# Performance work log

Measured on AMD Instinct MI355X. Metric: run time of the kernel, lower is better.

The kernel has to match this reference:

```python
import jax, jax.numpy as jnp
import numpy as np

B, S, D = 2, 1024, 1024
NH = 8
QK = 512   # qk_dim = 0.5 * D
V = 1024   # v_dim = 1.0 * D
DQK = QK // NH   # 64
DHV = V // NH    # 128
CAP = 15.0       # gate_soft_cap
NORM_EPS = 1e-6
DENOM_EPS = 1e-6


def soft_cap(x, cap):
    return cap * jnp.tanh(x / cap)


def setup_inputs() -> dict:
    key = jax.random.key(0)
    ks = jax.random.split(key, 8)
    s = 0.02
    return {
        "x": jax.random.normal(ks[0], (B, S, D), jnp.float32),
        "Wq": jax.random.normal(ks[1], (QK, D), jnp.float32) * s,
        "Wk": jax.random.normal(ks[2], (QK, D), jnp.float32) * s,
        "Wv": jax.random.normal(ks[3], (V, D), jnp.float32) * s,
        "Wog": jax.random.normal(ks[4], (V, D), jnp.float32) * s,
        "Wi": jax.random.normal(ks[5], (NH, D), jnp.float32) * s,
        "bi": jnp.zeros((NH,), jnp.float32),
        "Wf": jax.random.normal(ks[6], (NH, D), jnp.float32) * s,
        "bf": jnp.ones((NH,), jnp.float32),  # positive forget bias
        "gamma": jnp.ones((V,), jnp.float32),
        "Wout": jax.random.normal(ks[7], (D, V), jnp.float32) * s,
    }


def _mlstm_recurrent(q, k, v, i_pre, f_pre):
    # q,k: [B,S,NH,DQK]; v: [B,S,NH,DHV]; i_pre,f_pre: [B,S,NH]
    f_log = jax.nn.log_sigmoid(f_pre)
    q_s = q * (DQK ** -0.5)
    # move time to leading axis for scan
    xs = (jnp.moveaxis(q_s, 1, 0), jnp.moveaxis(k, 1, 0), jnp.moveaxis(v, 1, 0),
          jnp.moveaxis(i_pre, 1, 0), jnp.moveaxis(f_log, 1, 0))
    C0 = jnp.zeros((B, NH, DQK, DHV), q.dtype)
    n0 = jnp.zeros((B, NH, DQK), q.dtype)
    m0 = jnp.zeros((B, NH), q.dtype)

    def step(carry, xt):
        C, n, m = carry
        qt, kt, vt, it, ft = xt  # [B,NH,*]
        m_new = jnp.maximum(ft + m, it)                      # [B,NH]
        f_act = jnp.exp(ft + m - m_new)
        i_act = jnp.exp(it - m_new)
        C = f_act[..., None, None] * C + i_act[..., None, None] * (kt[..., :, None] * vt[..., None, :])
        n = f_act[..., None] * n + i_act[..., None] * kt
        h_num = jnp.einsum('bhd,bhdv->bhv', qt, C)
        qn = jnp.einsum('bhd,bhd->bh', qt, n)
        denom = jnp.maximum(jnp.abs(qn), jnp.exp(-m_new)) + DENOM_EPS
        h = h_num / denom[..., None]
        return (C, n, m_new), h

    (C, n, m), hs = jax.lax.scan(step, (C0, n0, m0), xs)
    return jnp.moveaxis(hs, 0, 1), (C, n, m)  # h: [B,S,NH,DHV]


def reference(x, Wq, Wk, Wv, Wog, Wi, bi, Wf, bf, gamma, Wout):
    q = (x @ Wq.T).reshape(B, S, NH, DQK)
    k = (x @ Wk.T).reshape(B, S, NH, DQK)
    v = (x @ Wv.T).reshape(B, S, NH, DHV)
    o_pre = x @ Wog.T                                  # [B,S,V]
    i_pre = soft_cap(x @ Wi.T + bi, CAP)               # [B,S,NH]
    f_pre = soft_cap(x @ Wf.T + bf, CAP)               # [B,S,NH]

    h, _state = _mlstm_recurrent(q, k, v, i_pre, f_pre)  # [B,S,NH,DHV]

    # multi-head layernorm over head dim, float32 reductions
    h32 = h.astype(jnp.float32)
    mu = jnp.mean(h32, axis=-1, keepdims=True)
    var = jnp.mean(jnp.square(h32 - mu), axis=-1, keepdims=True)
    h_norm = ((h32 - mu) * jax.lax.rsqrt(var + NORM_EPS)).astype(h.dtype)
    h_norm = h_norm * gamma.reshape(NH, DHV)
    h_norm = h_norm.reshape(B, S, V)

    h_out = jax.nn.sigmoid(o_pre) * h_norm
    y = h_out @ Wout.T
    return y
```

## Files before the change

### kernel.cpp

```cpp
#include <hip/hip_runtime.h>
#include <hip/hip_bf16.h>
#include <math.h>

typedef __bf16 bf16x8 __attribute__((ext_vector_type(8)));
typedef float f32x4 __attribute__((ext_vector_type(4)));

#define NB 2
#define NS 1024
#define ND 1024
#define NH 8
#define NQK 512
#define NV 1024
#define DQK 64
#define DHV 128
#define CHUNK 64
#define NCHUNK 16

#define GLDS16(g, l) __builtin_amdgcn_global_load_lds((const __attribute__((address_space(1))) void*)(g), (__attribute__((address_space(3))) void*)(l), 16, 0, 0)

static __device__ __forceinline__ void split_bf16(float v, __bf16& hi, __bf16& lo) {
  hi = (__bf16)v;
  lo = (__bf16)(v - (float)hi);
}

__global__ __launch_bounds__(256) void cvt_all(const float* __restrict__ x,
    const float* __restrict__ wq, const float* __restrict__ wk,
    const float* __restrict__ wv, const float* __restrict__ wog,
    const float* __restrict__ wout,
    __bf16* __restrict__ xb, __bf16* __restrict__ wb, __bf16* __restrict__ wob) {
  long i = (long)blockIdx.x * 256 + threadIdx.x;
  const float* src; __bf16* dst;
  if (i < 524288)        { src = x    + i*4;                    dst = xb  + i*4; }
  else if (i < 655360)   { long j = i -  524288; src = wq  + j*4; dst = wb + j*4; }
  else if (i < 786432)   { long j = i -  655360; src = wk  + j*4; dst = wb +  524288 + j*4; }
  else if (i < 1048576)  { long j = i -  786432; src = wv  + j*4; dst = wb + 1048576 + j*4; }
  else if (i < 1310720)  { long j = i - 1048576; src = wog + j*4; dst = wb + 2097152 + j*4; }
  else                   { long j = i - 1310720; src = wout+ j*4; dst = wob + j*4; }
  float4 v = *(const float4*)src;
  __bf16 o[4];
  o[0] = (__bf16)v.x; o[1] = (__bf16)v.y; o[2] = (__bf16)v.z; o[3] = (__bf16)v.w;
  *(short4*)dst = *(const short4*)o;
}

__global__ __launch_bounds__(256) void gemm_bt(const __bf16* __restrict__ A,
                                               const __bf16* __restrict__ Bm,
                                               float* __restrict__ C,
                                               int M, int N, int K) {
  __shared__ __bf16 smA[128 * 64];
  __shared__ __bf16 smB[128 * 64];
  const int tid = threadIdx.x;
  const int m0 = blockIdx.y * 128;
  const int n0 = blockIdx.x * 128;
  const int wid = tid >> 6, lane = tid & 63;
  const int wm = (wid >> 1) * 64, wn = (wid & 1) * 64;
  const int fr = lane & 15;
  const int g  = lane >> 4;
  f32x4 acc[4][4] = {};
  for (int kt = 0; kt < K; kt += 64) {
    #pragma unroll
    for (int i = 0; i < 4; ++i) {
      const int sbase = i * 256 + wid * 64;
      const int s = sbase + lane;
      const int row = s >> 3;
      const int klog = (s & 7) ^ (row & 7);
      GLDS16(A  + (size_t)(m0 + row) * K + kt + klog * 8, smA + sbase * 8);
      GLDS16(Bm + (size_t)(n0 + row) * K + kt + klog * 8, smB + sbase * 8);
    }
    __syncthreads();
    #pragma unroll
    for (int kk = 0; kk < 2; ++kk) {
      const int kg = kk * 4 + g;
      bf16x8 af[4], bfv[4];
      #pragma unroll
      for (int f = 0; f < 4; ++f) {
        const int Ra = wm + f * 16 + fr;
        const int Rb = wn + f * 16 + fr;
        af[f]  = *(const bf16x8*)&smA[Ra * 64 + ((kg ^ (Ra & 7)) * 8)];
        bfv[f] = *(const bf16x8*)&smB[Rb * 64 + ((kg ^ (Rb & 7)) * 8)];
      }
      #pragma unroll
      for (int i = 0; i < 4; ++i)
        #pragma unroll
        for (int j = 0; j < 4; ++j)
          acc[i][j] = __builtin_amdgcn_mfma_f32_16x16x32_bf16(af[i], bfv[j], acc[i][j], 0, 0, 0);
    }
    __syncthreads();
  }
  const int orow = m0 + wm + g * 4;
  const int ocol = n0 + wn + fr;
  #pragma unroll
  for (int i = 0; i < 4; ++i)
    #pragma unroll
    for (int j = 0; j < 4; ++j)
      #pragma unroll
      for (int r = 0; r < 4; ++r)
        C[(size_t)(orow + i*16 + r) * N + (ocol + j*16)] = acc[i][j][r];
}

__global__ __launch_bounds__(256) void ifgate_kernel(const float* __restrict__ x,
    const float* __restrict__ Wi, const float* __restrict__ bi,
    const float* __restrict__ Wf, const float* __restrict__ bf_,
    float* __restrict__ icap, float* __restrict__ flog) {
  const int row = blockIdx.x;
  const int w = threadIdx.x >> 6;
  const int l = threadIdx.x & 63;
  const float* xr = x + (size_t)row * ND;
  float xv[16];
  #pragma unroll
  for (int t = 0; t < 16; ++t) xv[t] = xr[l + 64*t];
  for (int hh = 0; hh < 2; ++hh) {
    int h = w*2 + hh;
    const float* wi = Wi + (size_t)h * ND;
    const float* wf = Wf + (size_t)h * ND;
    float si = 0.f, sf = 0.f;
    #pragma unroll
    for (int t = 0; t < 16; ++t) {
      si += xv[t] * wi[l + 64*t];
      sf += xv[t] * wf[l + 64*t];
    }
    #pragma unroll
    for (int off = 32; off; off >>= 1) {
      si += __shfl_xor(si, off, 64);
      sf += __shfl_xor(sf, off, 64);
    }
    if (l == 0) {
      float ic = 15.f * tanhf((si + bi[h]) * (1.f/15.f));
      float fc = 15.f * tanhf((sf + bf_[h]) * (1.f/15.f));
      float fl = (fc >= 0.f) ? -log1pf(__expf(-fc)) : (fc - log1pf(__expf(fc)));
      icap[row*NH + h] = ic;
      flog[row*NH + h] = fl;
    }
  }
}

__global__ __launch_bounds__(64) void gates_kernel(const float* __restrict__ icap,
    const float* __restrict__ flog, float* __restrict__ g_g, float* __restrict__ a_g,
    float* __restrict__ m_g, float* __restrict__ m0g) {
  const int bh = blockIdx.x;
  const int b = bh >> 3, h = bh & 7;
  const int l = threadIdx.x;
  float m0 = 0.f;
  for (int c = 0; c < NCHUNK; ++c) {
    const int t = c*CHUNK + l;
    const int row = b*NS + t;
    float B = flog[row*NH + h];
    float iv = icap[row*NH + h];
    #pragma unroll
    for (int d = 1; d < 64; d <<= 1) {
      float o = __shfl_up(B, d, 64);
      if (l >= d) B += o;
    }
    float g = iv - B;
    float cm = g;
    #pragma unroll
    for (int d = 1; d < 64; d <<= 1) {
      float o = __shfl_up(cm, d, 64);
      if (l >= d) cm = fmaxf(cm, o);
    }
    float a = fmaxf(m0, cm);
    float m = B + a;
    const int idx = bh*NS + t;
    g_g[idx] = g; a_g[idx] = a; m_g[idx] = m;
    if (l == 0) m0g[bh*NCHUNK + c] = m0;
    m0 = __shfl(m, 63, 64);
  }
}

__global__ __launch_bounds__(256) void u_kernel(const float* __restrict__ P,
    const float* __restrict__ g_g, const float* __restrict__ a_g,
    float* __restrict__ Ug, float* __restrict__ Ung) {
  __shared__ float w_l[64];
  __shared__ float knP[4][64];
  __shared__ __bf16 ksT[64][72];
  __shared__ __bf16 vwT[128][72];
  const int task = blockIdx.x;
  const int bh = task >> 4, c = task & 15;
  const int b = bh >> 3, h = bh & 7;
  const int t = threadIdx.x;
  const int row0 = b*NS + c*CHUNK;
  if (t < 64) {
    const float aL = a_g[bh*NS + c*CHUNK + 63];
    w_l[t] = __expf(g_g[bh*NS + c*CHUNK + t] - aL);
  }
  __syncthreads();
  {
    const int d = t & 63, sh = t >> 6;
    const float* src = P + (size_t)(row0 + sh*16)*3072 + NQK + h*DQK + d;
    float kn = 0.f;
    __bf16 tmp[16];
    #pragma unroll
    for (int i = 0; i < 16; ++i) {
      float kv = src[(size_t)i * 3072];
      kn += kv * w_l[sh*16 + i];
      tmp[i] = (__bf16)kv;
    }
    *(float4*)&ksT[d][sh*16]     = *(const float4*)&tmp[0];
    *(float4*)&ksT[d][sh*16 + 8] = *(const float4*)&tmp[8];
    knP[sh][d] = kn;
  }
  {
    const int u = t & 127, sh2 = t >> 7;
    const float* src = P + (size_t)(row0 + sh2*32)*3072 + 2*NQK + h*DHV + u;
    #pragma unroll
    for (int q4 = 0; q4 < 4; ++q4) {
      __bf16 tmp[8];
      #pragma unroll
      for (int i = 0; i < 8; ++i) {
        int s = sh2*32 + q4*8 + i;
        tmp[i] = (__bf16)(src[(size_t)(q4*8 + i) * 3072] * w_l[s]);
      }
      *(float4*)&vwT[u][sh2*32 + q4*8] = *(const float4*)&tmp[0];
    }
  }
  __syncthreads();
  if (t < 64) Ung[task*64 + t] = knP[0][t] + knP[1][t] + knP[2][t] + knP[3][t];
  const int wid = t >> 6, lane = t & 63;
  const int fr = lane & 15, g = lane >> 4;
  f32x4 acc[8] = {};
  #pragma unroll
  for (int kk = 0; kk < 2; ++kk) {
    const int kg = kk*4 + g;
    bf16x8 af = *(const bf16x8*)&ksT[wid*16 + fr][kg*8];
    #pragma unroll
    for (int nt = 0; nt < 8; ++nt) {
      bf16x8 bv = *(const bf16x8*)&vwT[nt*16 + fr][kg*8];
      acc[nt] = __builtin_amdgcn_mfma_f32_16x16x32_bf16(af, bv, acc[nt], 0, 0, 0);
    }
  }
  float* ub = Ug + (size_t)task * 64 * 128;
  #pragma unroll
  for (int nt = 0; nt < 8; ++nt)
    #pragma unroll
    for (int r = 0; r < 4; ++r)
      ub[(size_t)(wid*16 + g*4 + r) * 128 + nt*16 + fr] = acc[nt][r];
}

__global__ __launch_bounds__(512) void statescan_kernel(const float* __restrict__ Ug,
    const float* __restrict__ Ung, const float* __restrict__ m0g,
    const float* __restrict__ a_g, float* __restrict__ C0g, float* __restrict__ n0g) {
  const int bx = blockIdx.x;
  const int bh = bx >> 4, part = bx & 15;
  const int e = part*512 + threadIdx.x;
  float scale[NCHUNK];
  #pragma unroll
  for (int c = 0; c < NCHUNK; ++c)
    scale[c] = __expf(m0g[bh*NCHUNK + c] - a_g[bh*NS + c*CHUNK + 63]);
  float val = 0.f;
  for (int c = 0; c < NCHUNK; ++c) {
    size_t idx = ((size_t)(bh*NCHUNK + c))*8192 + e;
    C0g[idx] = val;
    val = scale[c]*val + Ug[idx];
  }
  if (part == 0 && threadIdx.x < 64) {
    float nv = 0.f;
    for (int c = 0; c < NCHUNK; ++c) {
      int idx = (bh*NCHUNK + c)*64 + threadIdx.x;
      n0g[idx] = nv;
      nv = scale[c]*nv + Ung[idx];
    }
  }
}

__global__ __launch_bounds__(256) void intra_kernel(const float* __restrict__ P,
    const float* __restrict__ g_g, const float* __restrict__ a_g,
    const float* __restrict__ m_g, const float* __restrict__ m0g,
    const float* __restrict__ C0g, const float* __restrict__ n0g,
    const float* __restrict__ gamma, __bf16* __restrict__ hout) {
  __shared__ __bf16 q_hi[32][72], q_lo[32][72];
  __shared__ __bf16 kvreg[2*64*72];
  __shared__ __bf16 c0T[128][72];
  __shared__ __bf16 Ps[32][72];
  __shared__ float g_l[64], n0_l[64], a_l[32], m_l[32], cI_l[32];
  __shared__ float qnA[2][32], qnI_l[32], lnS[2][32], lnQ[2][32];

  const int blk = blockIdx.x;
  const int task = blk >> 1, jhalf = blk & 1;
  const int bh = task >> 4, c = task & 15;
  const int b = bh >> 3, h = bh & 7;
  const int t = threadIdx.x;
  const int wid = t >> 6, lane = t & 63;
  const int fr = lane & 15, lg = lane >> 4;
  const int jt_local = wid >> 1, half = wid & 1;
  const int jtg = jhalf*2 + jt_local;
  const int row0 = b*NS + c*CHUNK;
  const int jrow0 = row0 + jhalf*32;
  __bf16* k_hi = kvreg;
  __bf16* k_lo = kvreg + 64*72;

  {
    const int r = t >> 3, c8 = (t & 7) * 8;
    const float* src = P + (size_t)(jrow0 + r)*3072 + h*DQK + c8;
    float4 v0 = *(const float4*)src;
    float4 v1 = *(const float4*)(src + 4);
    float vv[8] = {v0.x,v0.y,v0.z,v0.w,v1.x,v1.y,v1.z,v1.w};
    __bf16 hi8[8], lo8[8];
    #pragma unroll
    for (int i = 0; i < 8; ++i) split_bf16(vv[i]*0.125f, hi8[i], lo8[i]);
    *(float4*)&q_hi[r][c8] = *(const float4*)hi8;
    *(float4*)&q_lo[r][c8] = *(const float4*)lo8;
  }
  {
    const int r = t >> 2, c16 = (t & 3) * 16;
    const float* src = P + (size_t)(row0 + r)*3072 + NQK + h*DQK + c16;
    __bf16 hi8[16], lo8[16];
    #pragma unroll
    for (int i = 0; i < 16; ++i) split_bf16(src[i], hi8[i], lo8[i]);
    *(float4*)&k_hi[r*72 + c16]     = *(const float4*)&hi8[0];
    *(float4*)&k_hi[r*72 + c16 + 8] = *(const float4*)&hi8[8];
    *(float4*)&k_lo[r*72 + c16]     = *(const float4*)&lo8[0];
    *(float4*)&k_lo[r*72 + c16 + 8] = *(const float4*)&lo8[8];
  }
  {
    const int u = t & 127, dh = t >> 7;
    const float* src = C0g + (size_t)task*8192 + (size_t)(dh*32)*128 + u;
    #pragma unroll
    for (int q4 = 0; q4 < 4; ++q4) {
      __bf16 tmp[8];
      #pragma unroll
      for (int i = 0; i < 8; ++i) tmp[i] = (__bf16)src[(size_t)(q4*8 + i) * 128];
      *(float4*)&c0T[u][dh*32 + q4*8] = *(const float4*)tmp;
    }
  }
  const float m0v = m0g[bh*NCHUNK + c];
  if (t < 64) {
    g_l[t]  = g_g[bh*NS + c*CHUNK + t];
    n0_l[t] = n0g[task*64 + t];
  } else if (t < 96) {
    int jl = t - 64;
    float av = a_g[bh*NS + c*CHUNK + jhalf*32 + jl];
    a_l[jl] = av;
    m_l[jl] = m_g[bh*NS + c*CHUNK + jhalf*32 + jl];
    cI_l[jl] = __expf(m0v - av);
  }
  __syncthreads();

  float rsum[4] = {0.f, 0.f, 0.f, 0.f};
  for (int st = half; st < 4; st += 2) {
    if (st <= jtg) {
      f32x4 sacc = {};
      #pragma unroll
      for (int kk = 0; kk < 2; ++kk) {
        const int kg = kk*4 + lg;
        bf16x8 qh = *(const bf16x8*)&q_hi[jt_local*16 + fr][kg*8];
        bf16x8 ql = *(const bf16x8*)&q_lo[jt_local*16 + fr][kg*8];
        bf16x8 kh = *(const bf16x8*)&k_hi[(st*16 + fr)*72 + kg*8];
        bf16x8 kl = *(const bf16x8*)&k_lo[(st*16 + fr)*72 + kg*8];
        sacc = __builtin_amdgcn_mfma_f32_16x16x32_bf16(qh, kh, sacc, 0, 0, 0);
        sacc = __builtin_amdgcn_mfma_f32_16x16x32_bf16(qh, kl, sacc, 0, 0, 0);
        sacc = __builtin_amdgcn_mfma_f32_16x16x32_bf16(ql, kh, sacc, 0, 0, 0);
      }
      const int s_c = st*16 + fr;
      const float gs = g_l[s_c];
      #pragma unroll
      for (int r = 0; r < 4; ++r) {
        const int jl = jt_local*16 + lg*4 + r;
        const int j_c = jhalf*32 + jl;
        float w = (s_c <= j_c) ? __expf(gs - a_l[jl]) : 0.f;
        float p = sacc[r] * w;
        rsum[r] += p;
        Ps[jl][s_c] = (__bf16)p;
      }
    } else {
      #pragma unroll
      for (int r = 0; r < 4; ++r)
        Ps[jt_local*16 + lg*4 + r][st*16 + fr] = (__bf16)0.f;
    }
  }
  #pragma unroll
  for (int r = 0; r < 4; ++r) {
    #pragma unroll
    for (int off = 1; off < 16; off <<= 1) rsum[r] += __shfl_xor(rsum[r], off, 64);
  }
  if (fr == 0) {
    #pragma unroll
    for (int r = 0; r < 4; ++r) qnA[half][jt_local*16 + lg*4 + r] = rsum[r];
  }

  f32x4 acc[4] = {};
  #pragma unroll
  for (int kk = 0; kk < 2; ++kk) {
    const int kg = kk*4 + lg;
    bf16x8 aq = *(const bf16x8*)&q_hi[jt_local*16 + fr][kg*8];
    #pragma unroll
    for (int nt = 0; nt < 4; ++nt) {
      bf16x8 bc = *(const bf16x8*)&c0T[(half*4 + nt)*16 + fr][kg*8];
      acc[nt] = __builtin_amdgcn_mfma_f32_16x16x32_bf16(aq, bc, acc[nt], 0, 0, 0);
    }
  }
  {
    float ci4[4];
    #pragma unroll
    for (int r = 0; r < 4; ++r) ci4[r] = cI_l[jt_local*16 + lg*4 + r];
    #pragma unroll
    for (int nt = 0; nt < 4; ++nt)
      #pragma unroll
      for (int r = 0; r < 4; ++r) acc[nt][r] *= ci4[r];
  }
  if (half == 1) {
    const int jl = jt_local*16 + fr;
    const int d0 = lg*16;
    float s = 0.f;
    #pragma unroll
    for (int i = 0; i < 16; ++i) {
      float qv = (float)q_hi[jl][d0+i] + (float)q_lo[jl][d0+i];
      s += qv * n0_l[d0+i];
    }
    s += __shfl_xor(s, 16, 64);
    s += __shfl_xor(s, 32, 64);
    if (lane < 16) qnI_l[jl] = cI_l[jl] * s;
  }
  __syncthreads();

  {
    __bf16* vsT = kvreg;
    const int u = t & 127, sh = t >> 7;
    const float* src = P + (size_t)(row0 + sh*32)*3072 + 2*NQK + h*DHV + u;
    #pragma unroll
    for (int q4 = 0; q4 < 4; ++q4) {
      __bf16 tmp[8];
      #pragma unroll
      for (int i = 0; i < 8; ++i) tmp[i] = (__bf16)src[(size_t)(q4*8 + i) * 3072];
      *(float4*)&kvreg[u*72 + sh*32 + q4*8] = *(const float4*)tmp;
    }
  }
  __syncthreads();

  #pragma unroll
  for (int kk = 0; kk < 2; ++kk) {
    const int kg = kk*4 + lg;
    bf16x8 ap = *(const bf16x8*)&Ps[jt_local*16 + fr][kg*8];
    #pragma unroll
    for (int nt = 0; nt < 4; ++nt) {
      bf16x8 bv = *(const bf16x8*)&kvreg[((half*4 + nt)*16 + fr)*72 + kg*8];
      acc[nt] = __builtin_amdgcn_mfma_f32_16x16x32_bf16(ap, bv, acc[nt], 0, 0, 0);
    }
  }

  #pragma unroll
  for (int r = 0; r < 4; ++r) {
    const int jl = jt_local*16 + lg*4 + r;
    float qn = qnA[0][jl] + qnA[1][jl] + qnI_l[jl];
    float denom = fmaxf(fabsf(qn), __expf(-m_l[jl])) + 1e-6f;
    float rd = 1.f / denom;
    float s = 0.f, q2 = 0.f;
    #pragma unroll
    for (int nt = 0; nt < 4; ++nt) {
      float hv = acc[nt][r] * rd;
      acc[nt][r] = hv;
      s += hv; q2 += hv*hv;
    }
    #pragma unroll
    for (int off = 1; off < 16; off <<= 1) {
      s  += __shfl_xor(s,  off, 64);
      q2 += __shfl_xor(q2, off, 64);
    }
    if (fr == 0) { lnS[half][jl] = s; lnQ[half][jl] = q2; }
  }
  __syncthreads();

  #pragma unroll
  for (int r = 0; r < 4; ++r) {
    const int jl = jt_local*16 + lg*4 + r;
    float sm = lnS[0][jl] + lnS[1][jl];
    float sq = lnQ[0][jl] + lnQ[1][jl];
    float mu = sm * (1.f/128.f);
    float var = sq * (1.f/128.f) - mu*mu;
    float rstd = rsqrtf(var + 1e-6f);
    const int rowg = jrow0 + jl;
    #pragma unroll
    for (int nt = 0; nt < 4; ++nt) {
      const int u = (half*4 + nt)*16 + fr;
      float og = P[(size_t)rowg*3072 + 2048 + h*DHV + u];
      float sg = 1.f / (1.f + __expf(-og));
      float hn = (acc[nt][r] - mu) * rstd * gamma[h*DHV + u] * sg;
      hout[(size_t)rowg*NV + h*DHV + u] = (__bf16)hn;
    }
  }
}

extern "C" void kernel_launch(void* const* d_in, const int* in_sizes, int n_in,
                              void* d_out, int out_size, void* d_ws, size_t ws_size,
                              hipStream_t stream) {
  const float* x    = (const float*)d_in[0];
  const float* Wq   = (const float*)d_in[1];
  const float* Wk   = (const float*)d_in[2];
  const float* Wv   = (const float*)d_in[3];
  const float* Wog  = (const float*)d_in[4];
  const float* Wi   = (const float*)d_in[5];
  const float* bi   = (const float*)d_in[6];
  const float* Wf   = (const float*)d_in[7];
  const float* bf_  = (const float*)d_in[8];
  const float* gamma= (const float*)d_in[9];
  const float* Wout = (const float*)d_in[10];
  float* y = (float*)d_out;

  char* ws = (char*)d_ws;
  const size_t MB = 1u << 20;
  __bf16* xb   = (__bf16*)(ws + 0);
  __bf16* Wb   = (__bf16*)(ws + 4*MB);
  __bf16* Wob  = (__bf16*)(ws + 10*MB);
  float*  P    = (float*) (ws + 12*MB);
  float*  icap = (float*) (ws + 36*MB);
  float*  flog = (float*) (ws + 36*MB + 64*1024);
  float*  g_g  = (float*) (ws + 36*MB + 128*1024);
  float*  a_g  = (float*) (ws + 36*MB + 192*1024);
  float*  m_g  = (float*) (ws + 36*MB + 256*1024);
  float*  m0g  = (float*) (ws + 36*MB + 320*1024);
  float*  Ung  = (float*) (ws + 36*MB + 384*1024);
  float*  n0g  = (float*) (ws + 36*MB + 448*1024);
  float*  Ug   = (float*) (ws + 0);
  float*  C0g  = (float*) (ws + 37*MB);
  __bf16* houtb= (__bf16*)(ws + 45*MB);

  cvt_all<<<6144, 256, 0, stream>>>(x, Wq, Wk, Wv, Wog, Wout, xb, Wb, Wob);

  gemm_bt<<<dim3(3072/128, 2048/128), 256, 0, stream>>>(xb, Wb, P, 2048, 3072, 1024);

  ifgate_kernel<<<2048, 256, 0, stream>>>(x, Wi, bi, Wf, bf_, icap, flog);
  gates_kernel<<<16, 64, 0, stream>>>(icap, flog, g_g, a_g, m_g, m0g);
  u_kernel<<<256, 256, 0, stream>>>(P, g_g, a_g, Ug, Ung);
  statescan_kernel<<<256, 512, 0, stream>>>(Ug, Ung, m0g, a_g, C0g, n0g);
  intra_kernel<<<512, 256, 0, stream>>>(P, g_g, a_g, m_g, m0g, C0g, n0g, gamma, houtb);

  gemm_bt<<<dim3(1024/128, 2048/128), 256, 0, stream>>>(houtb, Wob, y, 2048, 1024, 1024);
}
```

Baseline: 177.5 us.

## Fuse projection epilogue into pre-split bf16 layouts, double-buffer GEMMs, XCD swizzle

Result: no change. 176.4 us (-0.7%).

```diff
diff --git a/kernel.cpp b/kernel.cpp
--- a/kernel.cpp
+++ b/kernel.cpp
@@ -21,6 +21,13 @@
 static __device__ __forceinline__ void split_bf16(float v, __bf16& hi, __bf16& lo) {
   hi = (__bf16)v;
   lo = (__bf16)(v - (float)hi);
+}
+
+static __device__ __forceinline__ int xcd_swz(int orig, int nwg) {
+  int q = nwg >> 3, r = nwg & 7;
+  int xcd = orig & 7, idx = orig >> 3;
+  int base = (xcd < r) ? xcd * (q + 1) : r * (q + 1) + (xcd - r) * q;
+  return base + idx;
 }
 
 __global__ __launch_bounds__(256) void cvt_all(const float* __restrict__ x,
@@ -42,31 +49,40 @@
   *(short4*)dst = *(const short4*)o;
 }
 
+#define GEMM_STAGE(Abuf, Bbuf, Aptr, Bptr, Krun, ktv)                         \
+  do {                                                                        \
+    _Pragma("unroll")                                                         \
+    for (int i_ = 0; i_ < 4; ++i_) {                                          \
+      const int sb_ = i_ * 256 + wid * 64;                                    \
+      const int s_ = sb_ + lane;                                              \
+      const int row_ = s_ >> 3;                                               \
+      const int klog_ = (s_ & 7) ^ (row_ & 7);                                \
+      GLDS16(Aptr + (size_t)(m0 + row_) * Krun + (ktv) * 64 + klog_ * 8, Abuf + sb_ * 8); \
+      GLDS16(Bptr + (size_t)(n0 + row_) * Krun + (ktv) * 64 + klog_ * 8, Bbuf + sb_ * 8); \
+    }                                                                         \
+  } while (0)
+
 __global__ __launch_bounds__(256) void gemm_bt(const __bf16* __restrict__ A,
                                                const __bf16* __restrict__ Bm,
                                                float* __restrict__ C,
-                                               int M, int N, int K) {
-  __shared__ __bf16 smA[128 * 64];
-  __shared__ __bf16 smB[128 * 64];
+                                               int M, int N, int K, int ntn, int nwg) {
+  __shared__ __bf16 smA[2][128 * 64];
+  __shared__ __bf16 smB[2][128 * 64];
+  const int wg = xcd_swz(blockIdx.x, nwg);
+  const int m0 = (wg / ntn) * 128;
+  const int n0 = (wg % ntn) * 128;
   const int tid = threadIdx.x;
-  const int m0 = blockIdx.y * 128;
-  const int n0 = blockIdx.x * 128;
   const int wid = tid >> 6, lane = tid & 63;
   const int wm = (wid >> 1) * 64, wn = (wid & 1) * 64;
   const int fr = lane & 15;
   const int g  = lane >> 4;
   f32x4 acc[4][4] = {};
-  for (int kt = 0; kt < K; kt += 64) {
-    #pragma unroll
-    for (int i = 0; i < 4; ++i) {
-      const int sbase = i * 256 + wid * 64;
-      const int s = sbase + lane;
-      const int row = s >> 3;
-      const int klog = (s & 7) ^ (row & 7);
-      GLDS16(A  + (size_t)(m0 + row) * K + kt + klog * 8, smA + sbase * 8);
-      GLDS16(Bm + (size_t)(n0 + row) * K + kt + klog * 8, smB + sbase * 8);
-    }
+  const int NT = K >> 6;
+  GEMM_STAGE(smA[0], smB[0], A, Bm, K, 0);
+  int cur = 0;
+  for (int kt = 0; kt < NT; ++kt) {
     __syncthreads();
+    if (kt + 1 < NT) GEMM_STAGE(smA[cur ^ 1], smB[cur ^ 1], A, Bm, K, kt + 1);
     #pragma unroll
     for (int kk = 0; kk < 2; ++kk) {
       const int kg = kk * 4 + g;
@@ -75,8 +91,8 @@
       for (int f = 0; f < 4; ++f) {
         const int Ra = wm + f * 16 + fr;
         const int Rb = wn + f * 16 + fr;
-        af[f]  = *(const bf16x8*)&smA[Ra * 64 + ((kg ^ (Ra & 7)) * 8)];
-        bfv[f] = *(const bf16x8*)&smB[Rb * 64 + ((kg ^ (Rb & 7)) * 8)];
+        af[f]  = *(const bf16x8*)&smA[cur][Ra * 64 + ((kg ^ (Ra & 7)) * 8)];
+        bfv[f] = *(const bf16x8*)&smB[cur][Rb * 64 + ((kg ^ (Rb & 7)) * 8)];
       }
       #pragma unroll
       for (int i = 0; i < 4; ++i)
@@ -84,7 +100,7 @@
         for (int j = 0; j < 4; ++j)
           acc[i][j] = __builtin_amdgcn_mfma_f32_16x16x32_bf16(af[i], bfv[j], acc[i][j], 0, 0, 0);
     }
-    __syncthreads();
+    cur ^= 1;
   }
   const int orow = m0 + wm + g * 4;
   const int ocol = n0 + wn + fr;
@@ -95,6 +111,114 @@
       #pragma unroll
       for (int r = 0; r < 4; ++r)
         C[(size_t)(orow + i*16 + r) * N + (ocol + j*16)] = acc[i][j][r];
+}
+
+__global__ __launch_bounds__(256) void gemm_proj(const __bf16* __restrict__ A,
+    const __bf16* __restrict__ Bm,
+    __bf16* __restrict__ qh, __bf16* __restrict__ ql,
+    __bf16* __restrict__ kh, __bf16* __restrict__ kl,
+    __bf16* __restrict__ kT, __bf16* __restrict__ vT,
+    _Float16* __restrict__ ogs) {
+  __shared__ __bf16 smA[2][128 * 64];
+  __shared__ __bf16 smB[2][128 * 64];
+  const int wg = xcd_swz(blockIdx.x, 384);
+  const int m0 = (wg / 24) * 128;
+  const int n0 = (wg % 24) * 128;
+  const int tid = threadIdx.x;
+  const int wid = tid >> 6, lane = tid & 63;
+  const int wm = (wid >> 1) * 64, wn = (wid & 1) * 64;
+  const int fr = lane & 15;
+  const int g  = lane >> 4;
+  f32x4 acc[4][4] = {};
+  GEMM_STAGE(smA[0], smB[0], A, Bm, 1024, 0);
+  int cur = 0;
+  for (int kt = 0; kt < 16; ++kt) {
+    __syncthreads();
+    if (kt + 1 < 16) GEMM_STAGE(smA[cur ^ 1], smB[cur ^ 1], A, Bm, 1024, kt + 1);
+    #pragma unroll
+    for (int kk = 0; kk < 2; ++kk) {
+      const int kg = kk * 4 + g;
+      bf16x8 af[4], bfv[4];
+      #pragma unroll
+      for (int f = 0; f < 4; ++f) {
+        const int Ra = wm + f * 16 + fr;
+        const int Rb = wn + f * 16 + fr;
+        af[f]  = *(const bf16x8*)&smA[cur][Ra * 64 + ((kg ^ (Ra & 7)) * 8)];
+        bfv[f] = *(const bf16x8*)&smB[cur][Rb * 64 + ((kg ^ (Rb & 7)) * 8)];
+      }
+      #pragma unroll
+      for (int i = 0; i < 4; ++i)
+        #pragma unroll
+        for (int j = 0; j < 4; ++j)
+          acc[i][j] = __builtin_amdgcn_mfma_f32_16x16x32_bf16(af[i], bfv[j], acc[i][j], 0, 0, 0);
+    }
+    cur ^= 1;
+  }
+  const int orow = m0 + wm + g * 4;
+  const int ocol = n0 + wn + fr;
+  const int rng = n0 >> 9;
+  if (rng == 0 || rng == 1) {
+    __bf16* Hb = (rng == 0) ? qh : kh;
+    __bf16* Lb = (rng == 0) ? ql : kl;
+    const float sc = (rng == 0) ? 0.125f : 1.0f;
+    #pragma unroll
+    for (int i = 0; i < 4; ++i)
+      #pragma unroll
+      for (int j = 0; j < 4; ++j) {
+        const int col = (ocol + j*16) & 511;
+        const int d = col & 63;
+        const int hb = col & ~63;
+        __bf16 t4[4];
+        #pragma unroll
+        for (int r = 0; r < 4; ++r) {
+          const int row = orow + i*16 + r;
+          float v = acc[i][j][r] * sc;
+          __bf16 hi, lo; split_bf16(v, hi, lo);
+          t4[r] = hi;
+          const int off = row*512 + hb + ((((d>>3) ^ (row&7))) << 3) + (d & 7);
+          Hb[off] = hi;
+          Lb[off] = lo;
+        }
+        if (rng == 1) {
+          const int row0r = orow + i*16;
+          const int bh = ((row0r >> 10) << 3) + (col >> 6);
+          const int c = (row0r >> 6) & 15;
+          const int s0 = (row0r & 63);
+          const int off = ((bh*16 + c)*64 + d)*64 + (((s0>>3) ^ (d&7)) << 3) + (s0 & 7);
+          *(short4*)&kT[off] = *(const short4*)t4;
+        }
+      }
+  } else if (rng == 2 || rng == 3) {
+    #pragma unroll
+    for (int i = 0; i < 4; ++i)
+      #pragma unroll
+      for (int j = 0; j < 4; ++j) {
+        const int col = (ocol + j*16) & 1023;
+        const int u = col & 127;
+        __bf16 t4[4];
+        #pragma unroll
+        for (int r = 0; r < 4; ++r) t4[r] = (__bf16)acc[i][j][r];
+        const int row0r = orow + i*16;
+        const int bh = ((row0r >> 10) << 3) + (col >> 7);
+        const int c = (row0r >> 6) & 15;
+        const int s0 = (row0r & 63);
+        const int off = ((bh*16 + c)*128 + u)*64 + (((s0>>3) ^ (u&7)) << 3) + (s0 & 7);
+        *(short4*)&vT[off] = *(const short4*)t4;
+      }
+  } else {
+    #pragma unroll
+    for (int i = 0; i < 4; ++i)
+      #pragma unroll
+      for (int j = 0; j < 4; ++j) {
+        const int col = (ocol + j*16) & 1023;
+        #pragma unroll
+        for (int r = 0; r < 4; ++r) {
+          const int row = orow + i*16 + r;
+          float sg = 1.f / (1.f + __expf(-acc[i][j][r]));
+          ogs[(size_t)row*1024 + col] = (_Float16)sg;
+        }
+      }
+  }
 }
 
 __global__ __launch_bounds__(256) void ifgate_kernel(const float* __restrict__ x,
@@ -166,90 +290,95 @@
   }
 }
 
-__global__ __launch_bounds__(256) void u_kernel(const float* __restrict__ P,
-    const float* __restrict__ g_g, const float* __restrict__ a_g,
-    float* __restrict__ Ug, float* __restrict__ Ung) {
+__global__ __launch_bounds__(256) void u_kernel(const __bf16* __restrict__ kT,
+    const __bf16* __restrict__ vT, const float* __restrict__ g_g,
+    const float* __restrict__ a_g, float* __restrict__ Ut, float* __restrict__ Ung) {
+  __shared__ __bf16 kts[64 * 64];
+  __shared__ __bf16 vts[128 * 64];
   __shared__ float w_l[64];
-  __shared__ float knP[4][64];
-  __shared__ __bf16 ksT[64][72];
-  __shared__ __bf16 vwT[128][72];
   const int task = blockIdx.x;
   const int bh = task >> 4, c = task & 15;
-  const int b = bh >> 3, h = bh & 7;
   const int t = threadIdx.x;
-  const int row0 = b*NS + c*CHUNK;
+  const int wid = t >> 6, lane = t & 63;
+  const int fr = lane & 15, g = lane >> 4;
   if (t < 64) {
     const float aL = a_g[bh*NS + c*CHUNK + 63];
     w_l[t] = __expf(g_g[bh*NS + c*CHUNK + t] - aL);
   }
+  {
+    const int sb = wid * 64;
+    #pragma unroll
+    for (int i = 0; i < 2; ++i) {
+      const int s = i*256 + sb + lane;
+      GLDS16(kT + (size_t)task*4096 + s*8, kts + (i*256 + sb)*8);
+    }
+    #pragma unroll
+    for (int i = 0; i < 4; ++i) {
+      const int s = i*256 + sb + lane;
+      GLDS16(vT + (size_t)task*8192 + s*8, vts + (i*256 + sb)*8);
+    }
+  }
   __syncthreads();
-  {
-    const int d = t & 63, sh = t >> 6;
-    const float* src = P + (size_t)(row0 + sh*16)*3072 + NQK + h*DQK + d;
-    float kn = 0.f;
-    __bf16 tmp[16];
-    #pragma unroll
-    for (int i = 0; i < 16; ++i) {
-      float kv = src[(size_t)i * 3072];
-      kn += kv * w_l[sh*16 + i];
-      tmp[i] = (__bf16)kv;
-    }
-    *(float4*)&ksT[d][sh*16]     = *(const float4*)&tmp[0];
-    *(float4*)&ksT[d][sh*16 + 8] = *(const float4*)&tmp[8];
-    knP[sh][d] = kn;
-  }
-  {
-    const int u = t & 127, sh2 = t >> 7;
-    const float* src = P + (size_t)(row0 + sh2*32)*3072 + 2*NQK + h*DHV + u;
-    #pragma unroll
-    for (int q4 = 0; q4 < 4; ++q4) {
-      __bf16 tmp[8];
-      #pragma unroll
-      for (int i = 0; i < 8; ++i) {
-        int s = sh2*32 + q4*8 + i;
-        tmp[i] = (__bf16)(src[(size_t)(q4*8 + i) * 3072] * w_l[s]);
-      }
-      *(float4*)&vwT[u][sh2*32 + q4*8] = *(const float4*)&tmp[0];
-    }
-  }
-  __syncthreads();
-  if (t < 64) Ung[task*64 + t] = knP[0][t] + knP[1][t] + knP[2][t] + knP[3][t];
-  const int wid = t >> 6, lane = t & 63;
-  const int fr = lane & 15, g = lane >> 4;
   f32x4 acc[8] = {};
   #pragma unroll
   for (int kk = 0; kk < 2; ++kk) {
     const int kg = kk*4 + g;
-    bf16x8 af = *(const bf16x8*)&ksT[wid*16 + fr][kg*8];
+    const int Ra = wid*16 + fr;
+    bf16x8 afr = *(const bf16x8*)&kts[Ra*64 + ((kg ^ (Ra & 7)) * 8)];
+    bf16x8 afw;
+    #pragma unroll
+    for (int j = 0; j < 8; ++j) afw[j] = (__bf16)((float)afr[j] * w_l[kg*8 + j]);
     #pragma unroll
     for (int nt = 0; nt < 8; ++nt) {
-      bf16x8 bv = *(const bf16x8*)&vwT[nt*16 + fr][kg*8];
-      acc[nt] = __builtin_amdgcn_mfma_f32_16x16x32_bf16(af, bv, acc[nt], 0, 0, 0);
-    }
-  }
-  float* ub = Ug + (size_t)task * 64 * 128;
-  #pragma unroll
-  for (int nt = 0; nt < 8; ++nt)
-    #pragma unroll
-    for (int r = 0; r < 4; ++r)
-      ub[(size_t)(wid*16 + g*4 + r) * 128 + nt*16 + fr] = acc[nt][r];
-}
-
-__global__ __launch_bounds__(512) void statescan_kernel(const float* __restrict__ Ug,
+      const int Rb = nt*16 + fr;
+      bf16x8 bv = *(const bf16x8*)&vts[Rb*64 + ((kg ^ (Rb & 7)) * 8)];
+      acc[nt] = __builtin_amdgcn_mfma_f32_16x16x32_bf16(afw, bv, acc[nt], 0, 0, 0);
+    }
+  }
+  float* ub = Ut + (size_t)task * 8192;
+  #pragma unroll
+  for (int nt = 0; nt < 8; ++nt) {
+    const int u = nt*16 + fr;
+    *(f32x4*)&ub[u*64 + wid*16 + g*4] = acc[nt];
+  }
+  if (t < 64) {
+    float s = 0.f;
+    #pragma unroll
+    for (int blk = 0; blk < 8; ++blk) {
+      bf16x8 kv = *(const bf16x8*)&kts[t*64 + ((blk ^ (t & 7)) * 8)];
+      #pragma unroll
+      for (int j = 0; j < 8; ++j) s += (float)kv[j] * w_l[blk*8 + j];
+    }
+    Ung[task*64 + t] = s;
+  }
+}
+
+__global__ __launch_bounds__(512) void statescan_kernel(const float* __restrict__ Ut,
     const float* __restrict__ Ung, const float* __restrict__ m0g,
-    const float* __restrict__ a_g, float* __restrict__ C0g, float* __restrict__ n0g) {
-  const int bx = blockIdx.x;
-  const int bh = bx >> 4, part = bx & 15;
-  const int e = part*512 + threadIdx.x;
+    const float* __restrict__ a_g, __bf16* __restrict__ C0T, float* __restrict__ n0g) {
+  const int bh = blockIdx.x >> 1, part = blockIdx.x & 1;
+  const int e8 = part*512 + threadIdx.x;
+  const int u = e8 >> 3, d8 = e8 & 7;
+  const int dsto = u*64 + ((d8 ^ (u & 7)) << 3);
+  const int srco = u*64 + d8*8;
   float scale[NCHUNK];
   #pragma unroll
   for (int c = 0; c < NCHUNK; ++c)
     scale[c] = __expf(m0g[bh*NCHUNK + c] - a_g[bh*NS + c*CHUNK + 63]);
-  float val = 0.f;
+  float val[8] = {};
   for (int c = 0; c < NCHUNK; ++c) {
-    size_t idx = ((size_t)(bh*NCHUNK + c))*8192 + e;
-    C0g[idx] = val;
-    val = scale[c]*val + Ug[idx];
+    const size_t base = ((size_t)(bh*NCHUNK + c)) * 8192;
+    __bf16 o[8];
+    #pragma unroll
+    for (int j = 0; j < 8; ++j) o[j] = (__bf16)val[j];
+    *(float4*)&C0T[base + dsto] = *(const float4*)o;
+    f32x4 u0 = *(const f32x4*)&Ut[base + srco];
+    f32x4 u1 = *(const f32x4*)&Ut[base + srco + 4];
+    #pragma unroll
+    for (int j = 0; j < 4; ++j) {
+      val[j]   = scale[c]*val[j]   + u0[j];
+      val[j+4] = scale[c]*val[j+4] + u1[j];
+    }
   }
   if (part == 0 && threadIdx.x < 64) {
     float nv = 0.f;
@@ -261,15 +390,20 @@
   }
 }
 
-__global__ __launch_bounds__(256) void intra_kernel(const float* __restrict__ P,
+__global__ __launch_bounds__(256) void intra_kernel(
+    const __bf16* __restrict__ qh, const __bf16* __restrict__ ql,
+    const __bf16* __restrict__ kh, const __bf16* __restrict__ kl,
+    const __bf16* __restrict__ vT, const __bf16* __restrict__ C0T,
+    const _Float16* __restrict__ ogs,
     const float* __restrict__ g_g, const float* __restrict__ a_g,
     const float* __restrict__ m_g, const float* __restrict__ m0g,
-    const float* __restrict__ C0g, const float* __restrict__ n0g,
+    const float* __restrict__ n0g,
     const float* __restrict__ gamma, __bf16* __restrict__ hout) {
-  __shared__ __bf16 q_hi[32][72], q_lo[32][72];
-  __shared__ __bf16 kvreg[2*64*72];
-  __shared__ __bf16 c0T[128][72];
-  __shared__ __bf16 Ps[32][72];
+  __shared__ __bf16 qh_s[32*64], ql_s[32*64];
+  __shared__ __bf16 kh_s[64*64], kl_s[64*64];
+  __shared__ __bf16 vt_s[128*64];
+  __shared__ __bf16 c0_s[128*64];
+  __shared__ __bf16 Ps[32*72];
   __shared__ float g_l[64], n0_l[64], a_l[32], m_l[32], cI_l[32];
   __shared__ float qnA[2][32], qnI_l[32], lnS[2][32], lnQ[2][32];
 
@@ -284,41 +418,29 @@
   const int jtg = jhalf*2 + jt_local;
   const int row0 = b*NS + c*CHUNK;
   const int jrow0 = row0 + jhalf*32;
-  __bf16* k_hi = kvreg;
-  __bf16* k_lo = kvreg + 64*72;
 
   {
-    const int r = t >> 3, c8 = (t & 7) * 8;
-    const float* src = P + (size_t)(jrow0 + r)*3072 + h*DQK + c8;
-    float4 v0 = *(const float4*)src;
-    float4 v1 = *(const float4*)(src + 4);
-    float vv[8] = {v0.x,v0.y,v0.z,v0.w,v1.x,v1.y,v1.z,v1.w};
-    __bf16 hi8[8], lo8[8];
-    #pragma unroll
-    for (int i = 0; i < 8; ++i) split_bf16(vv[i]*0.125f, hi8[i], lo8[i]);
-    *(float4*)&q_hi[r][c8] = *(const float4*)hi8;
-    *(float4*)&q_lo[r][c8] = *(const float4*)lo8;
-  }
-  {
-    const int r = t >> 2, c16 = (t & 3) * 16;
-    const float* src = P + (size_t)(row0 + r)*3072 + NQK + h*DQK + c16;
-    __bf16 hi8[16], lo8[16];
-    #pragma unroll
-    for (int i = 0; i < 16; ++i) split_bf16(src[i], hi8[i], lo8[i]);
-    *(float4*)&k_hi[r*72 + c16]     = *(const float4*)&hi8[0];
-    *(float4*)&k_hi[r*72 + c16 + 8] = *(const float4*)&hi8[8];
-    *(float4*)&k_lo[r*72 + c16]     = *(const float4*)&lo8[0];
-    *(float4*)&k_lo[r*72 + c16 + 8] = *(const float4*)&lo8[8];
-  }
-  {
-    const int u = t & 127, dh = t >> 7;
-    const float* src = C0g + (size_t)task*8192 + (size_t)(dh*32)*128 + u;
-    #pragma unroll
-    for (int q4 = 0; q4 < 4; ++q4) {
-      __bf16 tmp[8];
-      #pragma unroll
-      for (int i = 0; i < 8; ++i) tmp[i] = (__bf16)src[(size_t)(q4*8 + i) * 128];
-      *(float4*)&c0T[u][dh*32 + q4*8] = *(const float4*)tmp;
+    const int sb = wid * 64;
+    {
+      const int s = sb + lane;
+      const int r = s >> 3, bk = s & 7;
+      const size_t go = (size_t)(jrow0 + r)*512 + h*64 + bk*8;
+      GLDS16(qh + go, qh_s + sb*8);
+      GLDS16(ql + go, ql_s + sb*8);
+    }
+    #pragma unroll
+    for (int i = 0; i < 2; ++i) {
+      const int s = i*256 + sb + lane;
+      const int r = s >> 3, bk = s & 7;
+      const size_t go = (size_t)(row0 + r)*512 + h*64 + bk*8;
+      GLDS16(kh + go, kh_s + (i*256 + sb)*8);
+      GLDS16(kl + go, kl_s + (i*256 + sb)*8);
+    }
+    #pragma unroll
+    for (int i = 0; i < 4; ++i) {
+      const int s = i*256 + sb + lane;
+      GLDS16(vT  + (size_t)task*8192 + s*8, vt_s + (i*256 + sb)*8);
+      GLDS16(C0T + (size_t)task*8192 + s*8, c0_s + (i*256 + sb)*8);
     }
   }
   const float m0v = m0g[bh*NCHUNK + c];
@@ -341,13 +463,15 @@
       #pragma unroll
       for (int kk = 0; kk < 2; ++kk) {
         const int kg = kk*4 + lg;
-        bf16x8 qh = *(const bf16x8*)&q_hi[jt_local*16 + fr][kg*8];
-        bf16x8 ql = *(const bf16x8*)&q_lo[jt_local*16 + fr][kg*8];
-        bf16x8 kh = *(const bf16x8*)&k_hi[(st*16 + fr)*72 + kg*8];
-        bf16x8 kl = *(const bf16x8*)&k_lo[(st*16 + fr)*72 + kg*8];
-        sacc = __builtin_amdgcn_mfma_f32_16x16x32_bf16(qh, kh, sacc, 0, 0, 0);
-        sacc = __builtin_amdgcn_mfma_f32_16x16x32_bf16(qh, kl, sacc, 0, 0, 0);
-        sacc = __builtin_amdgcn_mfma_f32_16x16x32_bf16(ql, kh, sacc, 0, 0, 0);
+        const int Ra = jt_local*16 + fr;
+        const int Rb = st*16 + fr;
+        bf16x8 qhv = *(const bf16x8*)&qh_s[Ra*64 + ((kg ^ (Ra&7))*8)];
+        bf16x8 qlv = *(const bf16x8*)&ql_s[Ra*64 + ((kg ^ (Ra&7))*8)];
+        bf16x8 khv = *(const bf16x8*)&kh_s[Rb*64 + ((kg ^ (Rb&7))*8)];
+        bf16x8 klv = *(const bf16x8*)&kl_s[Rb*64 + ((kg ^ (Rb&7))*8)];
+        sacc = __builtin_amdgcn_mfma_f32_16x16x32_bf16(qhv, khv, sacc, 0, 0, 0);
+        sacc = __builtin_amdgcn_mfma_f32_16x16x32_bf16(qhv, klv, sacc, 0, 0, 0);
+        sacc = __builtin_amdgcn_mfma_f32_16x16x32_bf16(qlv, khv, sacc, 0, 0, 0);
       }
       const int s_c = st*16 + fr;
       const float gs = g_l[s_c];
@@ -358,12 +482,12 @@
         float w = (s_c <= j_c) ? __expf(gs - a_l[jl]) : 0.f;
         float p = sacc[r] * w;
         rsum[r] += p;
-        Ps[jl][s_c] = (__bf16)p;
+        Ps[jl*72 + s_c] = (__bf16)p;
       }
     } else {
       #pragma unroll
       for (int r = 0; r < 4; ++r)
-        Ps[jt_local*16 + lg*4 + r][st*16 + fr] = (__bf16)0.f;
+        Ps[(jt_local*16 + lg*4 + r)*72 + st*16 + fr] = (__bf16)0.f;
     }
   }
   #pragma unroll
@@ -380,10 +504,12 @@
   #pragma unroll
   for (int kk = 0; kk < 2; ++kk) {
     const int kg = kk*4 + lg;
-    bf16x8 aq = *(const bf16x8*)&q_hi[jt_local*16 + fr][kg*8];
+    const int Ra = jt_local*16 + fr;
+    bf16x8 aq = *(const bf16x8*)&qh_s[Ra*64 + ((kg ^ (Ra&7))*8)];
     #pragma unroll
     for (int nt = 0; nt < 4; ++nt) {
-      bf16x8 bc = *(const bf16x8*)&c0T[(half*4 + nt)*16 + fr][kg*8];
+      const int Rb = (half*4 + nt)*16 + fr;
+      bf16x8 bc = *(const bf16x8*)&c0_s[Rb*64 + ((kg ^ (Rb&7))*8)];
       acc[nt] = __builtin_amdgcn_mfma_f32_16x16x32_bf16(aq, bc, acc[nt], 0, 0, 0);
     }
   }
@@ -398,12 +524,13 @@
   }
   if (half == 1) {
     const int jl = jt_local*16 + fr;
-    const int d0 = lg*16;
     float s = 0.f;
     #pragma unroll
     for (int i = 0; i < 16; ++i) {
-      float qv = (float)q_hi[jl][d0+i] + (float)q_lo[jl][d0+i];
-      s += qv * n0_l[d0+i];
+      const int d = lg*16 + i;
+      const int off = jl*64 + (((d>>3) ^ (jl&7)) << 3) + (d & 7);
+      float qv = (float)qh_s[off] + (float)ql_s[off];
+      s += qv * n0_l[d];
     }
     s += __shfl_xor(s, 16, 64);
     s += __shfl_xor(s, 32, 64);
@@ -411,27 +538,14 @@
   }
   __syncthreads();
 
-  {
-    __bf16* vsT = kvreg;
-    const int u = t & 127, sh = t >> 7;
-    const float* src = P + (size_t)(row0 + sh*32)*3072 + 2*NQK + h*DHV + u;
-    #pragma unroll
-    for (int q4 = 0; q4 < 4; ++q4) {
-      __bf16 tmp[8];
-      #pragma unroll
-      for (int i = 0; i < 8; ++i) tmp[i] = (__bf16)src[(size_t)(q4*8 + i) * 3072];
-      *(float4*)&kvreg[u*72 + sh*32 + q4*8] = *(const float4*)tmp;
-    }
-  }
-  __syncthreads();
-
   #pragma unroll
   for (int kk = 0; kk < 2; ++kk) {
     const int kg = kk*4 + lg;
-    bf16x8 ap = *(const bf16x8*)&Ps[jt_local*16 + fr][kg*8];
+    bf16x8 ap = *(const bf16x8*)&Ps[(jt_local*16 + fr)*72 + kg*8];
     #pragma unroll
     for (int nt = 0; nt < 4; ++nt) {
-      bf16x8 bv = *(const bf16x8*)&kvreg[((half*4 + nt)*16 + fr)*72 + kg*8];
+      const int Rb = (half*4 + nt)*16 + fr;
+      bf16x8 bv = *(const bf16x8*)&vt_s[Rb*64 + ((kg ^ (Rb&7))*8)];
       acc[nt] = __builtin_amdgcn_mfma_f32_16x16x32_bf16(ap, bv, acc[nt], 0, 0, 0);
     }
   }
@@ -470,8 +584,7 @@
     #pragma unroll
     for (int nt = 0; nt < 4; ++nt) {
       const int u = (half*4 + nt)*16 + fr;
-      float og = P[(size_t)rowg*3072 + 2048 + h*DHV + u];
-      float sg = 1.f / (1.f + __expf(-og));
+      float sg = (float)ogs[(size_t)rowg*1024 + h*DHV + u];
       float hn = (acc[nt][r] - mu) * rstd * gamma[h*DHV + u] * sg;
       hout[(size_t)rowg*NV + h*DHV + u] = (__bf16)hn;
     }
@@ -496,31 +609,38 @@
 
   char* ws = (char*)d_ws;
   const size_t MB = 1u << 20;
-  __bf16* xb   = (__bf16*)(ws + 0);
-  __bf16* Wb   = (__bf16*)(ws + 4*MB);
-  __bf16* Wob  = (__bf16*)(ws + 10*MB);
-  float*  P    = (float*) (ws + 12*MB);
-  float*  icap = (float*) (ws + 36*MB);
-  float*  flog = (float*) (ws + 36*MB + 64*1024);
-  float*  g_g  = (float*) (ws + 36*MB + 128*1024);
-  float*  a_g  = (float*) (ws + 36*MB + 192*1024);
-  float*  m_g  = (float*) (ws + 36*MB + 256*1024);
-  float*  m0g  = (float*) (ws + 36*MB + 320*1024);
-  float*  Ung  = (float*) (ws + 36*MB + 384*1024);
-  float*  n0g  = (float*) (ws + 36*MB + 448*1024);
-  float*  Ug   = (float*) (ws + 0);
-  float*  C0g  = (float*) (ws + 37*MB);
-  __bf16* houtb= (__bf16*)(ws + 45*MB);
+  __bf16*   xb   = (__bf16*)  (ws + 0);
+  __bf16*   Wb   = (__bf16*)  (ws + 4*MB);
+  __bf16*   Wob  = (__bf16*)  (ws + 10*MB);
+  __bf16*   qh   = (__bf16*)  (ws + 12*MB);
+  __bf16*   ql   = (__bf16*)  (ws + 14*MB);
+  __bf16*   kh   = (__bf16*)  (ws + 16*MB);
+  __bf16*   kl   = (__bf16*)  (ws + 18*MB);
+  __bf16*   kT   = (__bf16*)  (ws + 20*MB);
+  __bf16*   vT   = (__bf16*)  (ws + 22*MB);
+  _Float16* ogs  = (_Float16*)(ws + 26*MB);
+  float*    Ut   = (float*)   (ws + 30*MB);
+  __bf16*   C0T  = (__bf16*)  (ws + 38*MB);
+  float*    icap = (float*)   (ws + 42*MB);
+  float*    flog = (float*)   (ws + 42*MB + 64*1024);
+  float*    g_g  = (float*)   (ws + 42*MB + 128*1024);
+  float*    a_g  = (float*)   (ws + 42*MB + 192*1024);
+  float*    m_g  = (float*)   (ws + 42*MB + 256*1024);
+  float*    m0g  = (float*)   (ws + 42*MB + 320*1024);
+  float*    Ung  = (float*)   (ws + 42*MB + 384*1024);
+  float*    n0g  = (float*)   (ws + 42*MB + 448*1024);
+  __bf16*   houtb= (__bf16*)  (ws + 44*MB);
 
   cvt_all<<<6144, 256, 0, stream>>>(x, Wq, Wk, Wv, Wog, Wout, xb, Wb, Wob);
 
-  gemm_bt<<<dim3(3072/128, 2048/128), 256, 0, stream>>>(xb, Wb, P, 2048, 3072, 1024);
+  gemm_proj<<<384, 256, 0, stream>>>(xb, Wb, qh, ql, kh, kl, kT, vT, ogs);
 
   ifgate_kernel<<<2048, 256, 0, stream>>>(x, Wi, bi, Wf, bf_, icap, flog);
   gates_kernel<<<16, 64, 0, stream>>>(icap, flog, g_g, a_g, m_g, m0g);
-  u_kernel<<<256, 256, 0, stream>>>(P, g_g, a_g, Ug, Ung);
-  statescan_kernel<<<256, 512, 0, stream>>>(Ug, Ung, m0g, a_g, C0g, n0g);
-  intra_kernel<<<512, 256, 0, stream>>>(P, g_g, a_g, m_g, m0g, C0g, n0g, gamma, houtb);
-
-  gemm_bt<<<dim3(1024/128, 2048/128), 256, 0, stream>>>(houtb, Wob, y, 2048, 1024, 1024);
-}
+  u_kernel<<<256, 256, 0, stream>>>(kT, vT, g_g, a_g, Ut, Ung);
+  statescan_kernel<<<32, 512, 0, stream>>>(Ut, Ung, m0g, a_g, C0T, n0g);
+  intra_kernel<<<512, 256, 0, stream>>>(qh, ql, kh, kl, vT, C0T, ogs,
+                                        g_g, a_g, m_g, m0g, n0g, gamma, houtb);
+
+  gemm_bt<<<128, 256, 0, stream>>>(houtb, Wob, y, 2048, 1024, 1024, 8, 128);
+}
```
